# Kernel tuning notes

Measured on AMD Instinct MI355X. Metric: run time of the kernel, lower is better.

## Reference

```python
import jax, jax.numpy as jnp
import numpy as np

EPS = 1e-5
NEG_SLOPE = 0.2

def _conv1x1(x, w):
    # x: (B,C,N,K), w: (O,C) -> (B,O,N,K)
    return jnp.einsum('oc,bcnk->bonk', w, x)

def _bn(x, g, b, m, v):
    scale = g / jnp.sqrt(v + EPS)
    return x * scale[None, :, None, None] + (b - m * scale)[None, :, None, None]

def _lrelu(x):
    return jnp.where(x > 0, x, NEG_SLOPE * x)

def setup_inputs() -> dict:
    key = jax.random.key(0)
    specs = {
        'x': ((8, 6, 8192, 20), 'randn'),
        'trans_w': ((64, 6), 'randn'), 'trans_g': ((64,), 'rand'), 'trans_b': ((64,), 'randn'),
        'trans_m': ((64,), 'randn'), 'trans_v': ((64,), 'rand'),
        'pos_w1': ((64, 3), 'randn'), 'pos_g': ((64,), 'rand'), 'pos_b': ((64,), 'randn'),
        'pos_m': ((64,), 'randn'), 'pos_v': ((64,), 'rand'),
        'pos_w2': ((64, 64), 'randn'), 'pos_b2': ((64,), 'randn'),
        'gate_w1': ((16, 6), 'randn'), 'gate_g': ((16,), 'rand'), 'gate_b': ((16,), 'randn'),
        'gate_m': ((16,), 'randn'), 'gate_v': ((16,), 'rand'),
        'gate_w2': ((1, 16), 'randn'), 'gate_b2': ((1,), 'ones'),
        'attn_w1': ((16, 6), 'randn'), 'attn_g': ((16,), 'rand'), 'attn_b': ((16,), 'randn'),
        'attn_m': ((16,), 'randn'), 'attn_v': ((16,), 'rand'),
        'attn_w2': ((64, 16), 'randn'), 'attn_b2': ((64,), 'randn'),
    }
    out = {}
    for i, (name, (shape, fill)) in enumerate(specs.items()):
        k = jax.random.fold_in(key, i)
        if fill == 'randn':
            out[name] = jax.random.normal(k, shape, dtype=jnp.float32) * 0.1
        elif fill == 'rand':
            out[name] = jax.random.uniform(k, shape, dtype=jnp.float32)
        else:  # ones (gate bias init to 2.0 in original; scale ones)
            out[name] = jnp.ones(shape, dtype=jnp.float32) * 2.0
    return out

def reference(x, trans_w, trans_g, trans_b, trans_m, trans_v,
              pos_w1, pos_g, pos_b, pos_m, pos_v, pos_w2, pos_b2,
              gate_w1, gate_g, gate_b, gate_m, gate_v, gate_w2, gate_b2,
              attn_w1, attn_g, attn_b, attn_m, attn_v, attn_w2, attn_b2):
    in_channels = 3
    rel_pos = x[:, in_channels:in_channels + 3, :, :]  # (B,3,N,K)
    # pos_net: conv(3->C) + BN + LReLU + conv(C->C, bias)
    pos_h = _lrelu(_bn(_conv1x1(rel_pos, pos_w1), pos_g, pos_b, pos_m, pos_v))
    pos_enc = _conv1x1(pos_h, pos_w2) + pos_b2[None, :, None, None]
    # trans: conv(2*Cin->C) + BN + LReLU
    trans_feat = _lrelu(_bn(_conv1x1(x, trans_w), trans_g, trans_b, trans_m, trans_v)) + pos_enc
    # gate_net: conv(6->16)+BN+LReLU+conv(16->1,bias)+sigmoid (dropout=0 in eval)
    gate_h = _lrelu(_bn(_conv1x1(x, gate_w1), gate_g, gate_b, gate_m, gate_v))
    gate_map = jax.nn.sigmoid(_conv1x1(gate_h, gate_w2) + gate_b2[None, :, None, None])  # (B,1,N,K)
    clean_feat = trans_feat * gate_map
    # attn_net: conv(6->16)+BN+LReLU+conv(16->C,bias), then + pos_enc, softmax over K
    attn_h = _lrelu(_bn(_conv1x1(x, attn_w1), attn_g, attn_b, attn_m, attn_v))
    attn_logits = _conv1x1(attn_h, attn_w2) + attn_b2[None, :, None, None] + pos_enc
    attn_weights = jax.nn.softmax(attn_logits, axis=-1)
    out_attn = (trans_feat * attn_weights).sum(axis=-1)  # (B,C,N)
    out_max = clean_feat.max(axis=-1)                    # (B,C,N)
    return out_attn + out_max
```

## Files before the change

kernel.cpp:

```cpp
#include <hip/hip_runtime.h>
#include <math.h>

#define NEG 0.2f
#define EPSV 1e-5f

typedef _Float16 v8h __attribute__((ext_vector_type(8)));
typedef _Float16 v4h __attribute__((ext_vector_type(4)));
typedef _Float16 v2h __attribute__((ext_vector_type(2)));
typedef __fp16   f16x2 __attribute__((ext_vector_type(2)));
typedef float    v4f __attribute__((ext_vector_type(4)));

__device__ __forceinline__ float lrelu(float v) { return fmaxf(v, NEG * v); }
__device__ __forceinline__ v4f lrelu4(v4f v) {
    return __builtin_elementwise_max(v, v * NEG);
}
__device__ __forceinline__ v2h lreluh2(v2h v) {
    return __builtin_elementwise_max(v, v * (_Float16)NEG);
}

__device__ __forceinline__ v2h pk(float a, float b) {
    union { f16x2 i; v2h o; } u;
    u.i = __builtin_amdgcn_cvt_pkrtz(a, b);
    return u.o;
}

#define MFMA32(a, b, c) __builtin_amdgcn_mfma_f32_16x16x32_f16((a), (b), (c), 0, 0, 0)
#define MFMA16(a, b, c) __builtin_amdgcn_mfma_f32_16x16x16f16((a), (b), (c), 0, 0, 0)

__global__ __launch_bounds__(256, 3)
void gsl_mfma(const float* __restrict__ x,
              const float* __restrict__ trans_w, const float* __restrict__ trans_g,
              const float* __restrict__ trans_b, const float* __restrict__ trans_m,
              const float* __restrict__ trans_v,
              const float* __restrict__ pos_w1, const float* __restrict__ pos_g,
              const float* __restrict__ pos_b, const float* __restrict__ pos_m,
              const float* __restrict__ pos_v, const float* __restrict__ pos_w2,
              const float* __restrict__ pos_b2,
              const float* __restrict__ gate_w1, const float* __restrict__ gate_g,
              const float* __restrict__ gate_b, const float* __restrict__ gate_m,
              const float* __restrict__ gate_v, const float* __restrict__ gate_w2,
              const float* __restrict__ gate_b2,
              const float* __restrict__ attn_w1, const float* __restrict__ attn_g,
              const float* __restrict__ attn_b, const float* __restrict__ attn_m,
              const float* __restrict__ attn_v, const float* __restrict__ attn_w2,
              const float* __restrict__ attn_b2,
              float* __restrict__ out)
{
    __shared__ _Float16 WH[1920];
    __shared__ _Float16 W2L[5120];
    __shared__ float    PB2[64];
    __shared__ _Float16 PHB[4][2][1152];
    __shared__ _Float16 AHB[4][2][320];

    const int tid  = threadIdx.x;
    const int wv   = tid >> 6;
    const int lane = tid & 63;
    const int p    = lane & 15;
    const int q    = lane >> 4;

    const int b  = blockIdx.x >> 7;
    const int n0 = ((blockIdx.x & 127) << 6) | (wv << 4);
    const int n  = n0 | p;

    #pragma unroll
    for (int e = 0; e < 16; ++e) {
        int idx = tid * 16 + e;
        int t   = idx >> 9;
        int rem = idx & 511;
        int pp  = rem >> 5;
        int ii  = rem & 31;
        W2L[t * 640 + pp * 40 + ii] =
            (_Float16)pos_w2[((t >> 1) * 16 + pp) * 64 + (t & 1) * 32 + ii];
    }

    if (tid < 64) {
        const int c = tid;
        float sp = pos_g[c] * rsqrtf(pos_v[c] + EPSV);
        float bp = pos_b[c] - pos_m[c] * sp;
        _Float16* row = WH + (c >> 4) * 320 + (c & 15) * 20;
        for (int k = 0; k < 20; ++k) {
            float v = (k >= 3 && k < 6) ? pos_w1[c * 3 + (k - 3)] * sp
                                        : ((k == 6) ? bp : 0.f);
            row[k] = (_Float16)v;
        }
        PB2[c] = pos_b2[c];
    } else if (tid < 80) {
        const int j = tid - 64;
        float sa = attn_g[j] * rsqrtf(attn_v[j] + EPSV);
        float ba = attn_b[j] - attn_m[j] * sa;
        _Float16* row = WH + 1280 + j * 20;
        for (int k = 0; k < 20; ++k)
            row[k] = (_Float16)((k < 6) ? attn_w1[j * 6 + k] * sa
                                        : ((k == 6) ? ba : 0.f));
    } else if (tid < 96) {
        const int j = tid - 80;
        float sg = gate_g[j] * rsqrtf(gate_v[j] + EPSV);
        float bg = gate_b[j] - gate_m[j] * sg;
        _Float16* row = WH + 1600 + j * 20;
        for (int k = 0; k < 20; ++k)
            row[k] = (_Float16)((k < 6) ? gate_w1[j * 6 + k] * sg
                                        : ((k == 6) ? bg : 0.f));
    }

    v4h WTf[4], WA2f[4];
    #pragma unroll
    for (int mt = 0; mt < 4; ++mt) {
        const int ch = mt * 16 + p;
        #pragma unroll
        for (int i = 0; i < 4; ++i)
            WA2f[mt][i] = (_Float16)attn_w2[ch * 16 + q * 4 + i];
        float st = trans_g[ch] * rsqrtf(trans_v[ch] + EPSV);
        float bt = trans_b[ch] - trans_m[ch] * st;
        #pragma unroll
        for (int i = 0; i < 4; ++i) {
            int k = q * 4 + i;
            float v = (k < 6) ? trans_w[ch * 6 + k] * st : ((k == 6) ? bt : 0.f);
            WTf[mt][i] = (_Float16)v;
        }
    }
    float g2w[4];
    #pragma unroll
    for (int r = 0; r < 4; ++r) g2w[r] = gate_w2[4 * q + r];
    const float gb2v = gate_b2[0];

    __syncthreads();

    const _Float16* const WP1p = WH + p * 20 + q * 4;
    const _Float16* const WA1p = WH + 1280 + p * 20 + q * 4;
    const _Float16* const WG1p = WH + 1600 + p * 20 + q * 4;
    const _Float16* const W2Lp = W2L + p * 40 + q * 8;
    const float* const    PB2p = PB2 + 4 * q;

    _Float16* const PHbase = &PHB[wv][0][0];
    _Float16* const AHbase = &AHB[wv][0][0];

    const v4f zero = {0.f, 0.f, 0.f, 0.f};
    v4f den[4], num[4], cmx[4];
    #pragma unroll
    for (int mt = 0; mt < 4; ++mt) {
        den[mt] = zero; num[mt] = zero;
        cmx[mt] = (v4f){-3.4e38f, -3.4e38f, -3.4e38f, -3.4e38f};
    }

    const float* xb = x + ((size_t)(b * 6) * 8192 + n) * 20;
    const int hi = q & 1;

    float nx[6];
    #pragma unroll
    for (int c = 0; c < 6; ++c) nx[c] = xb[(size_t)c * 163840];

    v4h xv_cur;
    {
        float s0 = hi ? nx[4] : nx[0], s1 = hi ? nx[5] : nx[1];
        float s2 = hi ? 1.f : nx[2],   s3 = hi ? 0.f : nx[3];
        v2h lo = pk(s0, s1), hh = pk(s2, s3);
        xv_cur = (v4h){lo.x, lo.y, hh.x, hh.y};
    }
    #pragma unroll
    for (int c = 0; c < 6; ++c) nx[c] = xb[(size_t)c * 163840 + 1];

    {
        v4f php[4];
        #pragma unroll
        for (int mt = 0; mt < 4; ++mt)
            php[mt] = MFMA16(*(const v4h*)(WP1p + mt * 320), xv_cur, zero);
        v4f ahp = MFMA16(*(const v4h*)WA1p, xv_cur, zero);
        _Float16* PHW = PHbase + p * 72 + 4 * q;
        #pragma unroll
        for (int mt = 0; mt < 4; ++mt) {
            union { v4h v; v2h h[2]; } u;
            u.h[0] = lreluh2(pk(php[mt][0], php[mt][1]));
            u.h[1] = lreluh2(pk(php[mt][2], php[mt][3]));
            *(v4h*)(PHW + mt * 16) = u.v;
        }
        union { v4h v; v2h h[2]; } ua;
        ua.h[0] = lreluh2(pk(ahp[0], ahp[1]));
        ua.h[1] = lreluh2(pk(ahp[2], ahp[3]));
        *(v4h*)(AHbase + p * 20 + 4 * q) = ua.v;
    }

    #pragma unroll 1
    for (int k = 0; k < 20; ++k) {
        asm volatile("" ::: "memory");

        const int sel = k & 1;
        _Float16* PH = PHbase + sel * 1152;
        _Float16* AH = AHbase + sel * 320;
        v8h phf0 = *(const v8h*)(PH + p * 72 + 8 * q);
        v8h phf1 = *(const v8h*)(PH + p * 72 + 32 + 8 * q);
        v4h ahf  = *(const v4h*)(AH + p * 20 + 4 * q);

        v4h xv_nxt = xv_cur;
        if (k < 19) {
            float s0 = hi ? nx[4] : nx[0], s1 = hi ? nx[5] : nx[1];
            float s2 = hi ? 1.f : nx[2],   s3 = hi ? 0.f : nx[3];
            v2h lo = pk(s0, s1), hh = pk(s2, s3);
            xv_nxt = (v4h){lo.x, lo.y, hh.x, hh.y};
            const int kn = (k < 18) ? k + 2 : 19;
            #pragma unroll
            for (int c = 0; c < 6; ++c) nx[c] = xb[(size_t)c * 163840 + kn];

            v4f php[4];
            #pragma unroll
            for (int mt = 0; mt < 4; ++mt)
                php[mt] = MFMA16(*(const v4h*)(WP1p + mt * 320), xv_nxt, zero);
            v4f ahp = MFMA16(*(const v4h*)WA1p, xv_nxt, zero);
            _Float16* PHW = PHbase + (sel ^ 1) * 1152 + p * 72 + 4 * q;
            #pragma unroll
            for (int mt = 0; mt < 4; ++mt) {
                union { v4h v; v2h h[2]; } uu;
                uu.h[0] = lreluh2(pk(php[mt][0], php[mt][1]));
                uu.h[1] = lreluh2(pk(php[mt][2], php[mt][3]));
                *(v4h*)(PHW + mt * 16) = uu.v;
            }
            union { v4h v; v2h h[2]; } ua;
            ua.h[0] = lreluh2(pk(ahp[0], ahp[1]));
            ua.h[1] = lreluh2(pk(ahp[2], ahp[3]));
            *(v4h*)(AHbase + (sel ^ 1) * 320 + p * 20 + 4 * q) = ua.v;
        }

        v4f ghp = MFMA16(*(const v4h*)WG1p, xv_cur, zero);
        float ga = 0.f;
        #pragma unroll
        for (int r = 0; r < 4; ++r) ga += g2w[r] * lrelu(ghp[r]);
        ga += __shfl_xor(ga, 16);
        ga += __shfl_xor(ga, 32);
        const float gate = 1.f / (1.f + __expf(-(ga + gb2v)));

        #pragma unroll
        for (int mt = 0; mt < 4; ++mt) {
            v8h w2a = *(const v8h*)(W2Lp + (mt * 2 + 0) * 640);
            v8h w2b = *(const v8h*)(W2Lp + (mt * 2 + 1) * 640);
            v4f pe = MFMA32(w2a, phf0, *(const v4f*)(PB2p + mt * 16));
            pe = MFMA32(w2b, phf1, pe);
            v4f tfa = MFMA16(WTf[mt], xv_cur, zero);
            v4f tfv = lrelu4(tfa) + pe;
            pe = MFMA16(WA2f[mt], ahf, pe);
            v4f e;
            #pragma unroll
            for (int r = 0; r < 4; ++r) e[r] = __expf(pe[r]);
            den[mt] += e;
            num[mt] += tfv * e;
            cmx[mt] = __builtin_elementwise_max(cmx[mt], tfv * gate);
        }
        xv_cur = xv_nxt;
    }

    #pragma unroll
    for (int mt = 0; mt < 4; ++mt) {
        #pragma unroll
        for (int r = 0; r < 4; ++r) {
            const int ch = mt * 16 + 4 * q + r;
            out[((size_t)(b * 64 + ch)) * 8192 + n] =
                num[mt][r] / den[mt][r] + cmx[mt][r];
        }
    }
}

extern "C" void kernel_launch(void* const* d_in, const int* in_sizes, int n_in,
                              void* d_out, int out_size, void* d_ws, size_t ws_size,
                              hipStream_t stream) {
    const float* x       = (const float*)d_in[0];
    const float* trans_w = (const float*)d_in[1];
    const float* trans_g = (const float*)d_in[2];
    const float* trans_b = (const float*)d_in[3];
    const float* trans_m = (const float*)d_in[4];
    const float* trans_v = (const float*)d_in[5];
    const float* pos_w1  = (const float*)d_in[6];
    const float* pos_g   = (const float*)d_in[7];
    const float* pos_b   = (const float*)d_in[8];
    const float* pos_m   = (const float*)d_in[9];
    const float* pos_v   = (const float*)d_in[10];
    const float* pos_w2  = (const float*)d_in[11];
    const float* pos_b2  = (const float*)d_in[12];
    const float* gate_w1 = (const float*)d_in[13];
    const float* gate_g  = (const float*)d_in[14];
    const float* gate_b  = (const float*)d_in[15];
    const float* gate_m  = (const float*)d_in[16];
    const float* gate_v  = (const float*)d_in[17];
    const float* gate_w2 = (const float*)d_in[18];
    const float* gate_b2 = (const float*)d_in[19];
    const float* attn_w1 = (const float*)d_in[20];
    const float* attn_g  = (const float*)d_in[21];
    const float* attn_b  = (const float*)d_in[22];
    const float* attn_m  = (const float*)d_in[23];
    const float* attn_v  = (const float*)d_in[24];
    const float* attn_w2 = (const float*)d_in[25];
    const float* attn_b2 = (const float*)d_in[26];
    float* out = (float*)d_out;

    gsl_mfma<<<1024, 256, 0, stream>>>(
        x, trans_w, trans_g, trans_b, trans_m, trans_v,
        pos_w1, pos_g, pos_b, pos_m, pos_v, pos_w2, pos_b2,
        gate_w1, gate_g, gate_b, gate_m, gate_v, gate_w2, gate_b2,
        attn_w1, attn_g, attn_b, attn_m, attn_v, attn_w2, attn_b2,
        out);
}
```

Measured before the change: 175.1 us.

## Unroll K loop by two with float2 loads and MFMA gate reduction

Restructures the per-neighbor loop into pairs with fixed ping-pong LDS buffers, and loads x as float2 through four per-lane pointers instead of six scalar loads per step. The gate's 16->1 projection moves from a scalar dot product with cross-lane shuffles to an MFMA, and launch bounds rise to 4 blocks per CU. The aim is fewer global load instructions, no shuffles and more occupancy. The risk is register spills under the tighter bound and fp16 rounding in the gate reduction.

```diff
diff --git a/kernel.cpp b/kernel.cpp
--- a/kernel.cpp
+++ b/kernel.cpp
@@ -27,7 +27,7 @@
 #define MFMA32(a, b, c) __builtin_amdgcn_mfma_f32_16x16x32_f16((a), (b), (c), 0, 0, 0)
 #define MFMA16(a, b, c) __builtin_amdgcn_mfma_f32_16x16x16f16((a), (b), (c), 0, 0, 0)
 
-__global__ __launch_bounds__(256, 3)
+__global__ __launch_bounds__(256, 4)
 void gsl_mfma(const float* __restrict__ x,
               const float* __restrict__ trans_w, const float* __restrict__ trans_g,
               const float* __restrict__ trans_b, const float* __restrict__ trans_m,
@@ -102,7 +102,7 @@
                                         : ((k == 6) ? bg : 0.f));
     }
 
-    v4h WTf[4], WA2f[4];
+    v4h WTf[4], WA2f[4], WG2f;
     #pragma unroll
     for (int mt = 0; mt < 4; ++mt) {
         const int ch = mt * 16 + p;
@@ -118,9 +118,9 @@
             WTf[mt][i] = (_Float16)v;
         }
     }
-    float g2w[4];
-    #pragma unroll
-    for (int r = 0; r < 4; ++r) g2w[r] = gate_w2[4 * q + r];
+    #pragma unroll
+    for (int i = 0; i < 4; ++i)
+        WG2f[i] = (_Float16)gate_w2[4 * q + i];
     const float gb2v = gate_b2[0];
 
     __syncthreads();
@@ -133,6 +133,10 @@
 
     _Float16* const PHbase = &PHB[wv][0][0];
     _Float16* const AHbase = &AHB[wv][0][0];
+    _Float16* const PH0 = PHbase;
+    _Float16* const PH1 = PHbase + 1152;
+    _Float16* const AH0 = AHbase;
+    _Float16* const AH1 = AHbase + 320;
 
     const v4f zero = {0.f, 0.f, 0.f, 0.f};
     v4f den[4], num[4], cmx[4];
@@ -142,30 +146,25 @@
         cmx[mt] = (v4f){-3.4e38f, -3.4e38f, -3.4e38f, -3.4e38f};
     }
 
-    const float* xb = x + ((size_t)(b * 6) * 8192 + n) * 20;
     const int hi = q & 1;
-
-    float nx[6];
-    #pragma unroll
-    for (int c = 0; c < 6; ++c) nx[c] = xb[(size_t)c * 163840];
-
-    v4h xv_cur;
-    {
-        float s0 = hi ? nx[4] : nx[0], s1 = hi ? nx[5] : nx[1];
-        float s2 = hi ? 1.f : nx[2],   s3 = hi ? 0.f : nx[3];
-        v2h lo = pk(s0, s1), hh = pk(s2, s3);
-        xv_cur = (v4h){lo.x, lo.y, hh.x, hh.y};
-    }
-    #pragma unroll
-    for (int c = 0; c < 6; ++c) nx[c] = xb[(size_t)c * 163840 + 1];
-
-    {
+    const float* pA = x + ((size_t)(b * 6 + (hi ? 4 : 0)) * 8192 + n) * 20;
+    const float* pB = x + ((size_t)(b * 6 + (hi ? 5 : 1)) * 8192 + n) * 20;
+    const float* pC = x + ((size_t)(b * 6 + (hi ? 4 : 2)) * 8192 + n) * 20;
+    const float* pD = x + ((size_t)(b * 6 + (hi ? 5 : 3)) * 8192 + n) * 20;
+
+    auto mk = [&](float a, float bb, float cc, float dd) -> v4h {
+        v2h lo = pk(a, bb);
+        v2h hh = pk(cc, dd);
+        if (hi) { union { unsigned u; v2h h; } t; t.u = 0x00003C00u; hh = t.h; }
+        return (v4h){lo.x, lo.y, hh.x, hh.y};
+    };
+
+    auto PRODUCE = [&](v4h xv, _Float16* PHW, _Float16* AHW) {
         v4f php[4];
         #pragma unroll
         for (int mt = 0; mt < 4; ++mt)
-            php[mt] = MFMA16(*(const v4h*)(WP1p + mt * 320), xv_cur, zero);
-        v4f ahp = MFMA16(*(const v4h*)WA1p, xv_cur, zero);
-        _Float16* PHW = PHbase + p * 72 + 4 * q;
+            php[mt] = MFMA16(*(const v4h*)(WP1p + mt * 320), xv, zero);
+        v4f ahp = MFMA16(*(const v4h*)WA1p, xv, zero);
         #pragma unroll
         for (int mt = 0; mt < 4; ++mt) {
             union { v4h v; v2h h[2]; } u;
@@ -176,56 +175,16 @@
         union { v4h v; v2h h[2]; } ua;
         ua.h[0] = lreluh2(pk(ahp[0], ahp[1]));
         ua.h[1] = lreluh2(pk(ahp[2], ahp[3]));
-        *(v4h*)(AHbase + p * 20 + 4 * q) = ua.v;
-    }
-
-    #pragma unroll 1
-    for (int k = 0; k < 20; ++k) {
-        asm volatile("" ::: "memory");
-
-        const int sel = k & 1;
-        _Float16* PH = PHbase + sel * 1152;
-        _Float16* AH = AHbase + sel * 320;
-        v8h phf0 = *(const v8h*)(PH + p * 72 + 8 * q);
-        v8h phf1 = *(const v8h*)(PH + p * 72 + 32 + 8 * q);
-        v4h ahf  = *(const v4h*)(AH + p * 20 + 4 * q);
-
-        v4h xv_nxt = xv_cur;
-        if (k < 19) {
-            float s0 = hi ? nx[4] : nx[0], s1 = hi ? nx[5] : nx[1];
-            float s2 = hi ? 1.f : nx[2],   s3 = hi ? 0.f : nx[3];
-            v2h lo = pk(s0, s1), hh = pk(s2, s3);
-            xv_nxt = (v4h){lo.x, lo.y, hh.x, hh.y};
-            const int kn = (k < 18) ? k + 2 : 19;
-            #pragma unroll
-            for (int c = 0; c < 6; ++c) nx[c] = xb[(size_t)c * 163840 + kn];
-
-            v4f php[4];
-            #pragma unroll
-            for (int mt = 0; mt < 4; ++mt)
-                php[mt] = MFMA16(*(const v4h*)(WP1p + mt * 320), xv_nxt, zero);
-            v4f ahp = MFMA16(*(const v4h*)WA1p, xv_nxt, zero);
-            _Float16* PHW = PHbase + (sel ^ 1) * 1152 + p * 72 + 4 * q;
-            #pragma unroll
-            for (int mt = 0; mt < 4; ++mt) {
-                union { v4h v; v2h h[2]; } uu;
-                uu.h[0] = lreluh2(pk(php[mt][0], php[mt][1]));
-                uu.h[1] = lreluh2(pk(php[mt][2], php[mt][3]));
-                *(v4h*)(PHW + mt * 16) = uu.v;
-            }
-            union { v4h v; v2h h[2]; } ua;
-            ua.h[0] = lreluh2(pk(ahp[0], ahp[1]));
-            ua.h[1] = lreluh2(pk(ahp[2], ahp[3]));
-            *(v4h*)(AHbase + (sel ^ 1) * 320 + p * 20 + 4 * q) = ua.v;
-        }
-
-        v4f ghp = MFMA16(*(const v4h*)WG1p, xv_cur, zero);
-        float ga = 0.f;
-        #pragma unroll
-        for (int r = 0; r < 4; ++r) ga += g2w[r] * lrelu(ghp[r]);
-        ga += __shfl_xor(ga, 16);
-        ga += __shfl_xor(ga, 32);
-        const float gate = 1.f / (1.f + __expf(-(ga + gb2v)));
+        *(v4h*)AHW = ua.v;
+    };
+
+    auto CONSUME = [&](v4h xv, v8h phf0, v8h phf1, v4h ahf) {
+        v4f ghp = MFMA16(*(const v4h*)WG1p, xv, zero);
+        union { v4h v; v2h h[2]; } ug;
+        ug.h[0] = lreluh2(pk(ghp[0], ghp[1]));
+        ug.h[1] = lreluh2(pk(ghp[2], ghp[3]));
+        v4f gav = MFMA16(WG2f, ug.v, zero);
+        const float gate = 1.f / (1.f + __expf(-(gav[0] + gb2v)));
 
         #pragma unroll
         for (int mt = 0; mt < 4; ++mt) {
@@ -233,7 +192,7 @@
             v8h w2b = *(const v8h*)(W2Lp + (mt * 2 + 1) * 640);
             v4f pe = MFMA32(w2a, phf0, *(const v4f*)(PB2p + mt * 16));
             pe = MFMA32(w2b, phf1, pe);
-            v4f tfa = MFMA16(WTf[mt], xv_cur, zero);
+            v4f tfa = MFMA16(WTf[mt], xv, zero);
             v4f tfv = lrelu4(tfa) + pe;
             pe = MFMA16(WA2f[mt], ahf, pe);
             v4f e;
@@ -243,7 +202,45 @@
             num[mt] += tfv * e;
             cmx[mt] = __builtin_elementwise_max(cmx[mt], tfv * gate);
         }
-        xv_cur = xv_nxt;
+    };
+
+    float2 cA = *(const float2*)pA;
+    float2 cB = *(const float2*)pB;
+    float2 cC = *(const float2*)pC;
+    float2 cD = *(const float2*)pD;
+    v4h xvE = mk(cA.x, cB.x, cC.x, cD.x);
+    PRODUCE(xvE, PH0 + p * 72 + 4 * q, AH0 + p * 20 + 4 * q);
+
+    #pragma unroll 1
+    for (int g = 0; g < 10; ++g) {
+        asm volatile("" ::: "memory");
+
+        float2 nA = cA, nB = cB, nC = cC, nD = cD;
+        if (g < 9) {
+            const int o = 2 * g + 2;
+            nA = *(const float2*)(pA + o);
+            nB = *(const float2*)(pB + o);
+            nC = *(const float2*)(pC + o);
+            nD = *(const float2*)(pD + o);
+        }
+
+        v8h phf0 = *(const v8h*)(PH0 + p * 72 + 8 * q);
+        v8h phf1 = *(const v8h*)(PH0 + p * 72 + 32 + 8 * q);
+        v4h ahf  = *(const v4h*)(AH0 + p * 20 + 4 * q);
+        v4h xvO = mk(cA.y, cB.y, cC.y, cD.y);
+        PRODUCE(xvO, PH1 + p * 72 + 4 * q, AH1 + p * 20 + 4 * q);
+        CONSUME(xvE, phf0, phf1, ahf);
+
+        phf0 = *(const v8h*)(PH1 + p * 72 + 8 * q);
+        phf1 = *(const v8h*)(PH1 + p * 72 + 32 + 8 * q);
+        ahf  = *(const v4h*)(AH1 + p * 20 + 4 * q);
+        if (g < 9) {
+            xvE = mk(nA.x, nB.x, nC.x, nD.x);
+            PRODUCE(xvE, PH0 + p * 72 + 4 * q, AH0 + p * 20 + 4 * q);
+        }
+        CONSUME(xvO, phf0, phf1, ahf);
+
+        cA = nA; cB = nB; cC = nC; cD = nD;
     }
 
     #pragma unroll
```

Measured after the change: 410.6 us. 2.34x slower.
